# Kernel optimization log

Hardware: AMD Instinct MI355X
Metric: run time of the kernel (lower is better)

The kernel has to match this reference:

```python
import jax, jax.numpy as jnp
import numpy as np

B, D = 1024, 512   # batch, feature dim (input_shape[1])
K, NC = 256, 1     # output_dim, num_centers (mask broadcast requires NC==1)


def setup_inputs() -> dict:
    key = jax.random.key(0)
    k1, k2, k3 = jax.random.split(key, 3)
    x = jax.random.normal(k1, (B, D), dtype=jnp.float32)
    # w_mean params (keras Constant init in the original; randomized for a nontrivial test)
    means = jax.random.normal(k2, (K, NC, D), dtype=jnp.float32) * 0.1
    # w_rho params (keras 'uniform' init: U[-0.05, 0.05]); sigma = softplus(rho)
    rho = jax.random.uniform(k3, (K, NC, D), minval=-0.05, maxval=0.05, dtype=jnp.float32)
    return {"x": x, "means": means, "rho": rho}


def reference(x, means, rho):
    # sigma = log(1 + exp(rho)), computed in build()
    sigma = jnp.log1p(jnp.exp(rho))                      # (K, NC, D)
    # squared difference, broadcast over all classes/centers at once
    d2 = (x[None, None, :, :] - means[:, :, None, :]) ** 2   # (K, NC, B, D)
    sig2 = sigma * sigma                                  # (K, NC, D)
    # logits[idx*NC + c][b] = sum_d d2/2 * sigma^2
    logits = jnp.sum(d2 * (0.5 * sig2)[:, :, None, :], axis=-1)   # (K, NC, B)
    # gaussian activation: exp(-sum_d d2 / (2 sigma^2))
    G = jnp.exp(-jnp.sum(d2 / (2.0 * sig2)[:, :, None, :], axis=-1))  # (K, NC, B)
    # P = (max_c G * (NC+1) - sum_c G) / NC
    P = (jnp.max(G, axis=1) * (NC + 1) - jnp.sum(G, axis=1)) / NC     # (K, B)
    probs = P.T                                           # (B, K)
    # stack order in TF: idx-major, c-minor -> (B, K*NC)
    logits_bk = jnp.transpose(logits, (2, 0, 1))          # (B, K, NC)
    mask = (probs >= 0.0).astype(logits_bk.dtype)         # (B, K)
    out = logits_bk * mask[:, :, None]                    # broadcast over NC (==1)
    return out.reshape(B, K * NC)
```

## Files before the change

kernel.cpp:

```cpp
#include <hip/hip_runtime.h>


#define BB 1024
#define DD 512
#define KK 256
#define SS 4
#define DSL (DD / SS)
#define BT 64
#define KT 64
#define DC 32
#define LSTR 68

__global__ __launch_bounds__(256) void prep_kernel(const float* __restrict__ means,
                                                   const float* __restrict__ rho,
                                                   float* __restrict__ w,
                                                   float* __restrict__ a2,
                                                   float* __restrict__ c) {
    const int k = blockIdx.x;
    const int t = threadIdx.x;
    __shared__ float red[256];
    float csum = 0.f;
    for (int d = t; d < DD; d += 256) {
        const float r  = rho[k * DD + d];
        const float m  = means[k * DD + d];
        const float sp = log1pf(expf(r));
        const float wv = 0.5f * sp * sp;
        w[k * DD + d]  = wv;
        a2[k * DD + d] = -2.0f * wv * m;
        csum += wv * m * m;
    }
    red[t] = csum;
    __syncthreads();
    for (int off = 128; off > 0; off >>= 1) {
        if (t < off) red[t] += red[t + off];
        __syncthreads();
    }
    if (t == 0) c[k] = red[0];
}

__global__ __launch_bounds__(256) void main_kernel(const float* __restrict__ x,
                                                   const float* __restrict__ w,
                                                   const float* __restrict__ a2,
                                                   const float* __restrict__ c,
                                                   float* __restrict__ out) {
    __shared__ float xT[DC][LSTR];
    __shared__ float wT[DC][LSTR];
    __shared__ float aT[DC][LSTR];

    const int t  = threadIdx.x;
    const int tx = t & 15;
    const int ty = t >> 4;
    const int k0 = blockIdx.x * KT;
    const int b0 = blockIdx.y * BT;
    const int d0 = blockIdx.z * DSL;

    const int lr  = t >> 3;
    const int ld4 = (t & 7) * 4;

    float acc[4][4];
#pragma unroll
    for (int i = 0; i < 4; i++)
#pragma unroll
        for (int j = 0; j < 4; j++) acc[i][j] = 0.f;

    for (int dcBase = 0; dcBase < DSL; dcBase += DC) {
        const int dg = d0 + dcBase + ld4;
#pragma unroll
        for (int half = 0; half < 2; half++) {
            const int row = lr + half * 32;
            const float4 xv = *(const float4*)&x[(b0 + row) * DD + dg];
            xT[ld4 + 0][row] = xv.x;
            xT[ld4 + 1][row] = xv.y;
            xT[ld4 + 2][row] = xv.z;
            xT[ld4 + 3][row] = xv.w;
            const float4 wv = *(const float4*)&w[(k0 + row) * DD + dg];
            wT[ld4 + 0][row] = wv.x;
            wT[ld4 + 1][row] = wv.y;
            wT[ld4 + 2][row] = wv.z;
            wT[ld4 + 3][row] = wv.w;
            const float4 av = *(const float4*)&a2[(k0 + row) * DD + dg];
            aT[ld4 + 0][row] = av.x;
            aT[ld4 + 1][row] = av.y;
            aT[ld4 + 2][row] = av.z;
            aT[ld4 + 3][row] = av.w;
        }
        __syncthreads();

#pragma unroll
        for (int d = 0; d < DC; d++) {
            const float4 xv = *(const float4*)&xT[d][ty * 4];
            const float4 wv = *(const float4*)&wT[d][tx * 4];
            const float4 av = *(const float4*)&aT[d][tx * 4];
            const float xs[4] = {xv.x, xv.y, xv.z, xv.w};
            const float ws[4] = {wv.x, wv.y, wv.z, wv.w};
            const float as[4] = {av.x, av.y, av.z, av.w};
#pragma unroll
            for (int i = 0; i < 4; i++)
#pragma unroll
                for (int j = 0; j < 4; j++) {
                    const float tmp = fmaf(ws[j], xs[i], as[j]);
                    acc[i][j] = fmaf(tmp, xs[i], acc[i][j]);
                }
        }
        __syncthreads();
    }

    float cv[4] = {0.f, 0.f, 0.f, 0.f};
    if (blockIdx.z == 0) {
#pragma unroll
        for (int j = 0; j < 4; j++) cv[j] = c[k0 + tx * 4 + j];
    }
#pragma unroll
    for (int i = 0; i < 4; i++) {
        const int b = b0 + ty * 4 + i;
#pragma unroll
        for (int j = 0; j < 4; j++) {
            const int k = k0 + tx * 4 + j;
            atomicAdd(&out[b * KK + k], acc[i][j] + cv[j]);
        }
    }
}

extern "C" void kernel_launch(void* const* d_in, const int* in_sizes, int n_in,
                              void* d_out, int out_size, void* d_ws, size_t ws_size,
                              hipStream_t stream) {
    const float* x     = (const float*)d_in[0];
    const float* means = (const float*)d_in[1];
    const float* rho   = (const float*)d_in[2];
    float* out = (float*)d_out;

    float* w  = (float*)d_ws;
    float* a2 = w + KK * DD;
    float* c  = a2 + KK * DD;

    hipMemsetAsync(d_out, 0, (size_t)out_size * sizeof(float), stream);

    prep_kernel<<<KK, 256, 0, stream>>>(means, rho, w, a2, c);

    dim3 grid(KK / KT, BB / BT, SS);
    main_kernel<<<grid, 256, 0, stream>>>(x, w, a2, c, out);
}
```

Before: 85.59 us.

## Recast weighted distance as bf16 MFMA GEMM over concatenated [x^2, x] features

Rewrites the distance sum as a single GEMM over concatenated features [x^2, x] against [w, -2wm], packed to bf16, and computes it with 16x16x32 bf16 MFMA instructions. It drops the split-K atomics and the output memset, so each wave writes its 16x16 tile directly. The intent is to replace scalar FP32 FMA work with matrix-core throughput. In exchange it adds a separate x preprocessing pass and loses precision, since x^2 and the weights are rounded to bf16 and large-magnitude logits may drift from an FP32 reference.

```diff
diff --git a/kernel.cpp b/kernel.cpp
--- a/kernel.cpp
+++ b/kernel.cpp
@@ -1,32 +1,51 @@
 #include <hip/hip_runtime.h>
+#include <hip/hip_bf16.h>
 
 
 #define BB 1024
 #define DD 512
+#define DP 1024
 #define KK 256
-#define SS 4
-#define DSL (DD / SS)
-#define BT 64
-#define KT 64
-#define DC 32
-#define LSTR 68
 
-__global__ __launch_bounds__(256) void prep_kernel(const float* __restrict__ means,
-                                                   const float* __restrict__ rho,
-                                                   float* __restrict__ w,
-                                                   float* __restrict__ a2,
-                                                   float* __restrict__ c) {
+typedef __attribute__((ext_vector_type(8))) short bf16x8;
+typedef __attribute__((ext_vector_type(4))) float f32x4;
+typedef __attribute__((ext_vector_type(4))) unsigned short us4;
+
+static __device__ inline unsigned short f2bf(float f) {
+    __hip_bfloat16 h = __float2bfloat16(f);
+    return *reinterpret_cast<unsigned short*>(&h);
+}
+
+__global__ __launch_bounds__(256) void prep_x_kernel(const float* __restrict__ x,
+                                                     unsigned short* __restrict__ Xp) {
+    const int i = blockIdx.x * 256 + threadIdx.x;
+    const int b = i >> 7;
+    const int d4 = (i & 127) * 4;
+    const float4 xv = *(const float4*)&x[b * DD + d4];
+    us4 sq, ln;
+    sq.x = f2bf(xv.x * xv.x); sq.y = f2bf(xv.y * xv.y);
+    sq.z = f2bf(xv.z * xv.z); sq.w = f2bf(xv.w * xv.w);
+    ln.x = f2bf(xv.x); ln.y = f2bf(xv.y); ln.z = f2bf(xv.z); ln.w = f2bf(xv.w);
+    *(us4*)&Xp[b * DP + d4]      = sq;
+    *(us4*)&Xp[b * DP + DD + d4] = ln;
+}
+
+__global__ __launch_bounds__(256) void prep_w_kernel(const float* __restrict__ means,
+                                                     const float* __restrict__ rho,
+                                                     unsigned short* __restrict__ Wp,
+                                                     float* __restrict__ c) {
     const int k = blockIdx.x;
     const int t = threadIdx.x;
     __shared__ float red[256];
     float csum = 0.f;
+#pragma unroll
     for (int d = t; d < DD; d += 256) {
         const float r  = rho[k * DD + d];
         const float m  = means[k * DD + d];
         const float sp = log1pf(expf(r));
         const float wv = 0.5f * sp * sp;
-        w[k * DD + d]  = wv;
-        a2[k * DD + d] = -2.0f * wv * m;
+        Wp[k * DP + d]      = f2bf(wv);
+        Wp[k * DP + DD + d] = f2bf(-2.0f * wv * m);
         csum += wv * m * m;
     }
     red[t] = csum;
@@ -38,86 +57,38 @@
     if (t == 0) c[k] = red[0];
 }
 
-__global__ __launch_bounds__(256) void main_kernel(const float* __restrict__ x,
-                                                   const float* __restrict__ w,
-                                                   const float* __restrict__ a2,
+__global__ __launch_bounds__(256) void gemm_kernel(const unsigned short* __restrict__ Xp,
+                                                   const unsigned short* __restrict__ Wp,
                                                    const float* __restrict__ c,
                                                    float* __restrict__ out) {
-    __shared__ float xT[DC][LSTR];
-    __shared__ float wT[DC][LSTR];
-    __shared__ float aT[DC][LSTR];
+    const int lane = threadIdx.x & 63;
+    const int wave = threadIdx.x >> 6;
+    const int tile = blockIdx.x * 4 + wave;
+    const int kb = tile & 15;
+    const int bb = tile >> 4;
+    const int k0 = kb * 16;
+    const int b0 = bb * 16;
 
-    const int t  = threadIdx.x;
-    const int tx = t & 15;
-    const int ty = t >> 4;
-    const int k0 = blockIdx.x * KT;
-    const int b0 = blockIdx.y * BT;
-    const int d0 = blockIdx.z * DSL;
+    const int rc   = lane & 15;
+    const int quad = lane >> 4;
 
-    const int lr  = t >> 3;
-    const int ld4 = (t & 7) * 4;
+    const unsigned short* aRow = Xp + (b0 + rc) * DP + quad * 8;
+    const unsigned short* bRow = Wp + (k0 + rc) * DP + quad * 8;
 
-    float acc[4][4];
-#pragma unroll
-    for (int i = 0; i < 4; i++)
-#pragma unroll
-        for (int j = 0; j < 4; j++) acc[i][j] = 0.f;
-
-    for (int dcBase = 0; dcBase < DSL; dcBase += DC) {
-        const int dg = d0 + dcBase + ld4;
-#pragma unroll
-        for (int half = 0; half < 2; half++) {
-            const int row = lr + half * 32;
-            const float4 xv = *(const float4*)&x[(b0 + row) * DD + dg];
-            xT[ld4 + 0][row] = xv.x;
-            xT[ld4 + 1][row] = xv.y;
-            xT[ld4 + 2][row] = xv.z;
-            xT[ld4 + 3][row] = xv.w;
-            const float4 wv = *(const float4*)&w[(k0 + row) * DD + dg];
-            wT[ld4 + 0][row] = wv.x;
-            wT[ld4 + 1][row] = wv.y;
-            wT[ld4 + 2][row] = wv.z;
-            wT[ld4 + 3][row] = wv.w;
-            const float4 av = *(const float4*)&a2[(k0 + row) * DD + dg];
-            aT[ld4 + 0][row] = av.x;
-            aT[ld4 + 1][row] = av.y;
-            aT[ld4 + 2][row] = av.z;
-            aT[ld4 + 3][row] = av.w;
-        }
-        __syncthreads();
-
-#pragma unroll
-        for (int d = 0; d < DC; d++) {
-            const float4 xv = *(const float4*)&xT[d][ty * 4];
-            const float4 wv = *(const float4*)&wT[d][tx * 4];
-            const float4 av = *(const float4*)&aT[d][tx * 4];
-            const float xs[4] = {xv.x, xv.y, xv.z, xv.w};
-            const float ws[4] = {wv.x, wv.y, wv.z, wv.w};
-            const float as[4] = {av.x, av.y, av.z, av.w};
-#pragma unroll
-            for (int i = 0; i < 4; i++)
-#pragma unroll
-                for (int j = 0; j < 4; j++) {
-                    const float tmp = fmaf(ws[j], xs[i], as[j]);
-                    acc[i][j] = fmaf(tmp, xs[i], acc[i][j]);
-                }
-        }
-        __syncthreads();
+    f32x4 acc = {0.f, 0.f, 0.f, 0.f};
+#pragma unroll 4
+    for (int dk = 0; dk < DP; dk += 32) {
+        const bf16x8 a = *(const bf16x8*)(aRow + dk);
+        const bf16x8 b = *(const bf16x8*)(bRow + dk);
+        acc = __builtin_amdgcn_mfma_f32_16x16x32_bf16(a, b, acc, 0, 0, 0);
     }
 
-    float cv[4] = {0.f, 0.f, 0.f, 0.f};
-    if (blockIdx.z == 0) {
+    const int col = rc;
+    const int row0 = quad * 4;
+    const float cv = c[k0 + col];
 #pragma unroll
-        for (int j = 0; j < 4; j++) cv[j] = c[k0 + tx * 4 + j];
-    }
-#pragma unroll
-    for (int i = 0; i < 4; i++) {
-        const int b = b0 + ty * 4 + i;
-#pragma unroll
-        for (int j = 0; j < 4; j++) {
-            const int k = k0 + tx * 4 + j;
-            atomicAdd(&out[b * KK + k], acc[i][j] + cv[j]);
-        }
+    for (int r = 0; r < 4; r++) {
+        out[(b0 + row0 + r) * KK + (k0 + col)] = acc[r] + cv;
     }
 }
 
@@ -129,14 +100,11 @@
     const float* rho   = (const float*)d_in[2];
     float* out = (float*)d_out;
 
-    float* w  = (float*)d_ws;
-    float* a2 = w + KK * DD;
-    float* c  = a2 + KK * DD;
+    unsigned short* Xp = (unsigned short*)d_ws;
+    unsigned short* Wp = Xp + (size_t)BB * DP;
+    float* c = (float*)(Wp + (size_t)KK * DP);
 
-    hipMemsetAsync(d_out, 0, (size_t)out_size * sizeof(float), stream);
-
-    prep_kernel<<<KK, 256, 0, stream>>>(means, rho, w, a2, c);
-
-    dim3 grid(KK / KT, BB / BT, SS);
-    main_kernel<<<grid, 256, 0, stream>>>(x, w, a2, c, out);
+    prep_x_kernel<<<(BB * DD / 4) / 256, 256, 0, stream>>>(x, Xp);
+    prep_w_kernel<<<KK, 256, 0, stream>>>(means, rho, Wp, c);
+    gemm_kernel<<<256, 256, 0, stream>>>(Xp, Wp, c, out);
 }
```

Result: faster. 71.25 us (-16.8%).
